# Kernel optimization log

Measured on AMD Instinct MI355X. Metric: run time of the kernel, lower is better.

The kernel has to match this reference:

```python
import jax, jax.numpy as jnp
import numpy as np

B, K, M, MN = 256, 32, 64, 256
E, H, Q = 128, 128, 128
NE, NR, NNODES = 100000, 500, 256  # entities, relations, max_nodes


def setup_inputs() -> dict:
    key = jax.random.key(0)
    ks = jax.random.split(key, 24)
    f = lambda k, s: jax.random.normal(k, s, jnp.float32) * 0.05
    inp = {}
    inp['start_entities'] = jax.random.randint(ks[0], (B,), 0, NE)
    inp['aims'] = jax.random.randint(ks[1], (B, K), 0, NE)
    inp['node_pos'] = jnp.broadcast_to(jnp.arange(1, K + 1, dtype=jnp.int32), (B, K))
    inp['neighbor_nodes'] = jax.random.randint(ks[2], (B, K, M), 0, NNODES)
    inp['neighbor_relations'] = jax.random.randint(ks[3], (B, K, M), 0, NR)
    inp['neighbors_num'] = jax.random.randint(ks[4], (B, K), 0, M + 1)
    inp['currents'] = jax.random.randint(ks[5], (B,), 0, NNODES)
    inp['candidate_nodes'] = jax.random.randint(ks[6], (B, MN), 0, NNODES)
    inp['candidate_entities'] = jax.random.randint(ks[7], (B, MN), 0, NE)
    inp['candidate_relations'] = jax.random.randint(ks[8], (B, MN), 0, NR)
    inp['candidate_masks'] = jax.random.randint(ks[9], (B, MN), 0, 2).astype(bool)
    inp['entity_emb'] = f(ks[10], (NE, E))
    inp['relation_emb'] = f(ks[11], (NR, E))
    inp['hidden_W'] = f(ks[12], (H, E)); inp['hidden_b'] = f(ks[13], (H,))
    inp['pass_W'] = f(ks[14], (H, H + E)); inp['pass_b'] = f(ks[15], (H,))
    inp['nexthop_W'] = f(ks[16], (H, H + Q)); inp['nexthop_b'] = f(ks[17], (H,))
    inp['candidate_W'] = f(ks[18], (H, H + 2 * E)); inp['candidate_b'] = f(ks[19], (H,))
    inp['gate_W'] = f(ks[20], (1, H + Q)); inp['gate_b'] = f(ks[21], (1,))
    inp['query'] = f(ks[22], (B, Q))
    return inp


def _linear(x, W, b):
    return x @ W.T + b


def _lrelu(x):
    return jax.nn.leaky_relu(x, 0.01)  # torch LeakyReLU default


def _gather_nodes(node_emb, idx):
    # node_emb: (B, N+2, H), idx: (B, ...) -> (B, ..., H)
    b = node_emb.shape[0]
    g = jnp.take_along_axis(node_emb, idx.reshape(b, -1)[:, :, None], axis=1)
    return g.reshape(*idx.shape, node_emb.shape[-1])


def reference(start_entities, aims, node_pos, neighbor_nodes, neighbor_relations,
              neighbors_num, currents, candidate_nodes, candidate_entities,
              candidate_relations, candidate_masks, entity_emb, relation_emb,
              hidden_W, hidden_b, pass_W, pass_b, nexthop_W, nexthop_b,
              candidate_W, candidate_b, gate_W, gate_b, query):
    # ---- Agent.init ----
    node_emb = jnp.zeros((B, NNODES + 2, H), jnp.float32)
    init = _lrelu(_linear(entity_emb[start_entities], hidden_W, hidden_b))
    node_emb = node_emb.at[:, 0].set(init)
    # ---- Agent.aggregate: gather -> Linear -> masked mean -> scatter ----
    aim_e = entity_emb[aims]                                   # (B,K,E)
    nb_node = _gather_nodes(node_emb, neighbor_nodes)          # (B,K,M,H)
    nb_rel = relation_emb[neighbor_relations]                  # (B,K,M,E)
    nb = _linear(jnp.concatenate([nb_node, nb_rel], -1), pass_W, pass_b)  # pass_activation = identity
    keep = jnp.arange(M) < neighbors_num[:, :, None]           # (B,K,M)
    nb = jnp.where(keep[..., None], nb, 0.0)
    denom = (neighbors_num + (neighbors_num == 0)).astype(jnp.float32)
    agg = nb.sum(axis=2) / denom[..., None]                    # (B,K,H)
    upd = _lrelu(_linear(aim_e, hidden_W, hidden_b) + agg)
    node_emb = node_emb.at[jnp.arange(B)[:, None], node_pos].set(upd)
    # ---- Agent.next_hop ----
    cur = _gather_nodes(node_emb, currents)                    # (B,H)
    cur_cat = jnp.concatenate([cur, query], axis=1)            # (B,H+Q)
    state = _lrelu(_linear(cur_cat, nexthop_W, nexthop_b))     # (B,H)
    cnode = _gather_nodes(node_emb, candidate_nodes)           # (B,MN,H)
    cand = _lrelu(_linear(jnp.concatenate(
        [cnode, entity_emb[candidate_entities], relation_emb[candidate_relations]], -1),
        candidate_W, candidate_b))                             # (B,MN,H)
    thresh = _linear(cur_cat, gate_W, gate_b)                  # (B,1)
    scores = jnp.einsum('bh,bmh->bm', state, cand) / jnp.sqrt(jnp.float32(E))
    scores = jnp.where(candidate_masks, scores, jnp.float32(-100000.0))
    final_scores = jnp.concatenate([scores, thresh], axis=1)   # (B,MN+1)
    return final_scores
```

## Files before the change

kernel.cpp:

```cpp
#include <hip/hip_runtime.h>

#define B 256
#define K 32
#define M 64
#define MN 256
#define E 128
#define H 128
#define Q 128
#define NSLOT 258
#define CTILE 32
#define XPAD 392

typedef __attribute__((ext_vector_type(8))) short short8;
typedef __attribute__((ext_vector_type(4))) short short4b;
typedef __attribute__((ext_vector_type(4))) float f32x4;

__device__ __forceinline__ float lrelu(float x){ return x >= 0.f ? x : 0.01f*x; }

__device__ __forceinline__ unsigned short f2bf(float f){
    unsigned int u = __float_as_uint(f);
    unsigned int r = u + 0x7FFFu + ((u >> 16) & 1u);
    return (unsigned short)(r >> 16);
}

__device__ __forceinline__ short4b pack4(float4 v){
    short4b r;
    r.x = (short)f2bf(v.x); r.y = (short)f2bf(v.y);
    r.z = (short)f2bf(v.z); r.w = (short)f2bf(v.w);
    return r;
}

__global__ void k_prep(const int* __restrict__ start_ent, const int* __restrict__ node_pos,
                       const float* __restrict__ ent_emb,
                       const float* __restrict__ hW, const float* __restrict__ hb,
                       const float* __restrict__ passW, const float* __restrict__ candW,
                       int* __restrict__ map,
                       float* __restrict__ init_out, float* __restrict__ wninit_out,
                       unsigned short* __restrict__ Wf, unsigned short* __restrict__ Wcatf){
    int blk = blockIdx.x, t = threadIdx.x;
    if (blk < 256) {
        int b = blk;
        __shared__ float e[E];
        __shared__ float si[H];
        if (t < 128) e[t] = ent_emb[(long)start_ent[b]*E + t];
        __syncthreads();
        if (t < 128) {
            float acc = hb[t];
            #pragma unroll 8
            for (int j=0;j<E;j++) acc += hW[t*E+j]*e[j];
            float v = lrelu(acc);
            si[t] = v;
            init_out[b*H+t] = v;
        }
        __syncthreads();
        if (t < 128) {
            float acc2 = 0.f;
            #pragma unroll 8
            for (int j=0;j<H;j++) acc2 += passW[t*(H+E)+j]*si[j];
            wninit_out[b*H+t] = acc2;
        }
    } else if (blk < 512) {
        int b = blk - 256;
        for (int i=t;i<NSLOT;i+=256) map[b*NSLOT+i] = -2;
        __syncthreads();
        if (t==0) map[b*NSLOT+0] = -1;
        __syncthreads();
        if (t<K) map[b*NSLOT + node_pos[b*K+t]] = t;
    } else if (blk < 704) {
        int i = (blk-512)*256 + t;
        int j = i & 7;
        int l = (i >> 3) & 63;
        int ct = (i >> 9) & 1;
        int r = i >> 10;
        int ks = r % 12, w = r / 12;
        int row = w*32 + ct*16 + (l & 15);
        int col = ks*32 + (l >> 4)*8 + j;
        Wf[i] = f2bf(candW[row*384 + col]);
    } else {
        int i = (blk-704)*256 + t;
        int j = i & 7;
        int l = (i >> 3) & 63;
        int ct = (i >> 9) & 1;
        int r = i >> 10;
        int ks = r & 7, w = r >> 3;
        int row = w*32 + ct*16 + (l & 15);
        int col = ks*32 + (l >> 4)*8 + j;
        float v = (col < 128) ? passW[row*256 + 128 + col] : hW[row*128 + (col-128)];
        Wcatf[i] = f2bf(v);
    }
}

__global__ void k_gather(const int* __restrict__ aims, const int* __restrict__ nbr_nodes,
                         const int* __restrict__ nbr_rels, const int* __restrict__ nbr_num,
                         const float* __restrict__ ent_emb, const float* __restrict__ rel_emb,
                         unsigned short* __restrict__ Xg,
                         float* __restrict__ ab){
    int bk = blockIdx.x;
    int t = threadIdx.x;
    int num = nbr_num[bk];
    __shared__ int sidx[M];
    __shared__ int sc0;
    __shared__ float red[8][128];
    if (t < 64) sidx[t] = nbr_rels[(long)bk*M + t];
    if (t >= 64 && t < 128) {
        int m = t - 64;
        bool flag = (m < num) && (nbr_nodes[(long)bk*M + m] == 0);
        unsigned long long mask = __ballot(flag);
        if (m == 0) sc0 = (int)__popcll(mask);
    }
    if (t >= 128) {
        int d = t - 128;
        Xg[(long)bk*256 + 128 + d] = f2bf(ent_emb[(long)aims[bk]*E + d]);
    }
    __syncthreads();
    int mg = t >> 5, q = t & 31;
    float4 acc = {0.f,0.f,0.f,0.f};
    for (int m = mg; m < num; m += 8) {
        const float4 v = *(const float4*)&rel_emb[(long)sidx[m]*E + q*4];
        acc.x += v.x; acc.y += v.y; acc.z += v.z; acc.w += v.w;
    }
    red[mg][q*4+0] = acc.x; red[mg][q*4+1] = acc.y;
    red[mg][q*4+2] = acc.z; red[mg][q*4+3] = acc.w;
    __syncthreads();
    float denom = (float)(num > 0 ? num : 1);
    if (t < 128) {
        float s = 0.f;
        #pragma unroll
        for (int g=0; g<8; g++) s += red[g][t];
        Xg[(long)bk*256 + t] = f2bf(s / denom);
    }
    if (t == 0) {
        ab[bk*2+0] = (float)sc0 / denom;
        ab[bk*2+1] = (float)num / denom;
    }
}

__global__ void k_updg(const unsigned short* __restrict__ Xg, const float* __restrict__ ab,
                       const unsigned short* __restrict__ Wcatf,
                       const float* __restrict__ hb_, const float* __restrict__ passb,
                       const float* __restrict__ wninit,
                       float* __restrict__ upd){
    int b = blockIdx.x;
    int t = threadIdx.x;
    __shared__ __align__(16) unsigned short Xs[32][264];
    __shared__ float wni[128];
    __shared__ float sab[64];
    #pragma unroll
    for (int it = 0; it < 4; it++) {
        int idx = it*256 + t;
        int r = idx >> 5;
        int cc = (idx & 31) * 8;
        *(short8*)&Xs[r][cc] = *(const short8*)&Xg[((long)b*32 + r)*256 + cc];
    }
    if (t < 128) wni[t] = wninit[b*128 + t];
    else if (t < 192) sab[t-128] = ab[b*64 + (t-128)];

    int w    = t >> 6;
    int lane = t & 63;
    int l16  = lane & 15;
    int lhi  = lane >> 4;
    int hbase = w*32;

    short8 bw[8][2];
    #pragma unroll
    for (int ks = 0; ks < 8; ks++) {
        #pragma unroll
        for (int ct = 0; ct < 2; ct++)
            bw[ks][ct] = *(const short8*)&Wcatf[((((w*8+ks)*2+ct)*64) + lane)*8];
    }
    __syncthreads();

    f32x4 acc[2][2];
    #pragma unroll
    for (int rt=0;rt<2;rt++)
        #pragma unroll
        for (int ct=0;ct<2;ct++)
            acc[rt][ct] = (f32x4){0.f,0.f,0.f,0.f};

    #pragma unroll
    for (int ks = 0; ks < 8; ks++) {
        int kof = ks*32 + lhi*8;
        short8 a0 = *(const short8*)&Xs[l16][kof];
        short8 a1 = *(const short8*)&Xs[16 + l16][kof];
        acc[0][0] = __builtin_amdgcn_mfma_f32_16x16x32_bf16(a0, bw[ks][0], acc[0][0], 0, 0, 0);
        acc[0][1] = __builtin_amdgcn_mfma_f32_16x16x32_bf16(a0, bw[ks][1], acc[0][1], 0, 0, 0);
        acc[1][0] = __builtin_amdgcn_mfma_f32_16x16x32_bf16(a1, bw[ks][0], acc[1][0], 0, 0, 0);
        acc[1][1] = __builtin_amdgcn_mfma_f32_16x16x32_bf16(a1, bw[ks][1], acc[1][1], 0, 0, 0);
    }

    int h0 = hbase + l16, h1 = hbase + 16 + l16;
    float hb0 = hb_[h0], hb1 = hb_[h1];
    float pb0 = passb[h0], pb1 = passb[h1];
    float w0 = wni[h0],  w1 = wni[h1];
    #pragma unroll
    for (int rt=0; rt<2; rt++) {
        #pragma unroll
        for (int i=0;i<4;i++) {
            int r = rt*16 + 4*lhi + i;
            float al = sab[r*2], be = sab[r*2+1];
            upd[((long)b*32 + r)*128 + h0] = lrelu(hb0 + al*w0 + be*pb0 + acc[rt][0][i]);
            upd[((long)b*32 + r)*128 + h1] = lrelu(hb1 + al*w1 + be*pb1 + acc[rt][1][i]);
        }
    }
}

__global__ void k_state(const int* __restrict__ currents, const int* __restrict__ map,
                        const float* __restrict__ init, const float* __restrict__ upd,
                        const float* __restrict__ query,
                        const float* __restrict__ nW, const float* __restrict__ nb,
                        const float* __restrict__ gW, const float* __restrict__ gb,
                        float* __restrict__ state, float* __restrict__ out){
    int b = blockIdx.x, t = threadIdx.x;
    __shared__ float cc[H+Q];
    __shared__ float wsum[2];
    int mv = map[b*NSLOT + currents[b]];
    float cv = 0.f;
    if (mv == -1) cv = init[b*H+t];
    else if (mv >= 0) cv = upd[((long)b*K+mv)*H + t];
    cc[t] = cv;
    cc[H+t] = query[b*Q+t];
    __syncthreads();
    float acc = nb[t];
    #pragma unroll 8
    for (int j=0;j<H+Q;j++) acc += nW[t*(H+Q)+j]*cc[j];
    state[b*H+t] = lrelu(acc);
    float tv = gW[t]*cc[t] + gW[H+t]*cc[H+t];
    for (int off=32; off>0; off>>=1) tv += __shfl_down(tv, off);
    if ((t&63)==0) wsum[t>>6] = tv;
    __syncthreads();
    if (t==0) out[b*(MN+1) + MN] = wsum[0] + wsum[1] + gb[0];
}

__global__ void k_cand(const int* __restrict__ cnodes, const int* __restrict__ cents,
                       const int* __restrict__ crels, const int* __restrict__ cmask,
                       const int* __restrict__ map,
                       const float* __restrict__ init, const float* __restrict__ upd,
                       const float* __restrict__ ent_emb, const float* __restrict__ rel_emb,
                       const unsigned short* __restrict__ Wf, const float* __restrict__ cb,
                       const float* __restrict__ state,
                       float* __restrict__ out){
    int blk = blockIdx.x;
    int b  = blk >> 3;
    int c0 = (blk & 7) * CTILE;
    int t  = threadIdx.x;

    __shared__ __align__(16) unsigned short Xb[CTILE][XPAD];
    __shared__ float sscore[4][CTILE];
    __shared__ int sce[CTILE], scr[CTILE], smv[CTILE];

    if (t < CTILE) {
        int row = b*MN + c0 + t;
        int cn = cnodes[row];
        sce[t] = cents[row];
        scr[t] = crels[row];
        smv[t] = map[b*NSLOT + cn];
    }
    __syncthreads();

    {
        int c8 = t >> 5;
        int q  = t & 31;
        #pragma unroll
        for (int i = 0; i < 4; i++) {
            int c = i*8 + c8;
            int mv = smv[c];
            float4 nv = {0.f,0.f,0.f,0.f};
            if (mv == -1)      nv = *(const float4*)&init[b*H + q*4];
            else if (mv >= 0)  nv = *(const float4*)&upd[((long)b*K+mv)*H + q*4];
            float4 ev = *(const float4*)&ent_emb[(long)sce[c]*E + q*4];
            float4 rv = *(const float4*)&rel_emb[(long)scr[c]*E + q*4];
            *(short4b*)&Xb[c][q*4]        = pack4(nv);
            *(short4b*)&Xb[c][128 + q*4]  = pack4(ev);
            *(short4b*)&Xb[c][256 + q*4]  = pack4(rv);
        }
    }

    int w    = t >> 6;
    int lane = t & 63;
    int l16  = lane & 15;
    int lhi  = lane >> 4;

    short8 bw[12][2];
    #pragma unroll
    for (int ks = 0; ks < 12; ks++) {
        #pragma unroll
        for (int ct = 0; ct < 2; ct++)
            bw[ks][ct] = *(const short8*)&Wf[((((w*12+ks)*2+ct)*64) + lane)*8];
    }
    float s0 = state[b*H + w*32 + l16];
    float s1 = state[b*H + w*32 + 16 + l16];
    float cb0 = cb[w*32 + l16];
    float cb1 = cb[w*32 + 16 + l16];
    __syncthreads();

    f32x4 acc[2][2];
    #pragma unroll
    for (int rt=0;rt<2;rt++)
        #pragma unroll
        for (int ct=0;ct<2;ct++)
            acc[rt][ct] = (f32x4){0.f,0.f,0.f,0.f};

    #pragma unroll
    for (int ks = 0; ks < 12; ks++) {
        int kof = ks*32 + lhi*8;
        short8 a0 = *(const short8*)&Xb[l16][kof];
        short8 a1 = *(const short8*)&Xb[16 + l16][kof];
        acc[0][0] = __builtin_amdgcn_mfma_f32_16x16x32_bf16(a0, bw[ks][0], acc[0][0], 0, 0, 0);
        acc[0][1] = __builtin_amdgcn_mfma_f32_16x16x32_bf16(a0, bw[ks][1], acc[0][1], 0, 0, 0);
        acc[1][0] = __builtin_amdgcn_mfma_f32_16x16x32_bf16(a1, bw[ks][0], acc[1][0], 0, 0, 0);
        acc[1][1] = __builtin_amdgcn_mfma_f32_16x16x32_bf16(a1, bw[ks][1], acc[1][1], 0, 0, 0);
    }

    #pragma unroll
    for (int rt=0; rt<2; rt++) {
        float ps[4];
        #pragma unroll
        for (int i=0;i<4;i++)
            ps[i] = lrelu(acc[rt][0][i] + cb0)*s0 + lrelu(acc[rt][1][i] + cb1)*s1;
        #pragma unroll
        for (int msk=1; msk<16; msk<<=1) {
            #pragma unroll
            for (int i=0;i<4;i++) ps[i] += __shfl_xor(ps[i], msk);
        }
        if (l16 == 0) {
            #pragma unroll
            for (int i=0;i<4;i++)
                sscore[w][rt*16 + 4*lhi + i] = ps[i];
        }
    }
    __syncthreads();

    if (t < CTILE) {
        int row = b*MN + c0 + t;
        float s = (sscore[0][t] + sscore[1][t] + sscore[2][t] + sscore[3][t])
                  * 0.08838834764831845f;
        out[b*(MN+1) + c0 + t] = cmask[row] ? s : -100000.0f;
    }
}

extern "C" void kernel_launch(void* const* d_in, const int* in_sizes, int n_in,
                              void* d_out, int out_size, void* d_ws, size_t ws_size,
                              hipStream_t stream){
    (void)in_sizes; (void)n_in; (void)out_size; (void)ws_size;
    const int* start_entities      = (const int*)d_in[0];
    const int* aims                = (const int*)d_in[1];
    const int* node_pos            = (const int*)d_in[2];
    const int* neighbor_nodes      = (const int*)d_in[3];
    const int* neighbor_relations  = (const int*)d_in[4];
    const int* neighbors_num       = (const int*)d_in[5];
    const int* currents            = (const int*)d_in[6];
    const int* candidate_nodes     = (const int*)d_in[7];
    const int* candidate_entities  = (const int*)d_in[8];
    const int* candidate_relations = (const int*)d_in[9];
    const int* candidate_masks     = (const int*)d_in[10];
    const float* entity_emb   = (const float*)d_in[11];
    const float* relation_emb = (const float*)d_in[12];
    const float* hidden_W     = (const float*)d_in[13];
    const float* hidden_b     = (const float*)d_in[14];
    const float* pass_W       = (const float*)d_in[15];
    const float* pass_b       = (const float*)d_in[16];
    const float* nexthop_W    = (const float*)d_in[17];
    const float* nexthop_b    = (const float*)d_in[18];
    const float* candidate_W  = (const float*)d_in[19];
    const float* candidate_b  = (const float*)d_in[20];
    const float* gate_W       = (const float*)d_in[21];
    const float* gate_b       = (const float*)d_in[22];
    const float* query        = (const float*)d_in[23];
    float* out = (float*)d_out;

    float* ws     = (float*)d_ws;
    float* init   = ws;
    float* wninit = init + B*H;
    float* upd    = wninit + B*H;
    float* state  = upd + (long)B*K*H;
    float* ab     = state + B*H;
    int*   map    = (int*)(ab + B*K*2);
    unsigned short* Wf    = (unsigned short*)(map + B*NSLOT);
    unsigned short* Wcatf = Wf + 49152;
    unsigned short* Xg    = Wcatf + 32768;

    k_prep<<<832, 256, 0, stream>>>(start_entities, node_pos, entity_emb,
                                    hidden_W, hidden_b, pass_W, candidate_W,
                                    map, init, wninit, Wf, Wcatf);
    k_gather<<<B*K, 256, 0, stream>>>(aims, neighbor_nodes, neighbor_relations, neighbors_num,
                                      entity_emb, relation_emb, Xg, ab);
    k_updg<<<B, 256, 0, stream>>>(Xg, ab, Wcatf, hidden_b, pass_b, wninit, upd);
    k_state<<<B, 128, 0, stream>>>(currents, map, init, upd, query,
                                   nexthop_W, nexthop_b, gate_W, gate_b, state, out);
    k_cand<<<B*(MN/CTILE), 256, 0, stream>>>(candidate_nodes, candidate_entities,
                                             candidate_relations, candidate_masks,
                                             map, init, upd, entity_emb, relation_emb,
                                             Wf, candidate_b, state, out);
}
```

Before: 55.90 us.

## Fuse gather into prep kernel and compute next-hop state inside candidate kernel

Merges the prep and neighbor-gather kernels into one launch. The separate next-hop state kernel is removed: each candidate block recomputes the state vector with bf16 MFMA against a pre-packed nexthop weight, and the block with c0==0 writes the gate threshold. This cuts two launches and the state round-trip through global memory. In exchange the state matvec is done redundantly in all 8 candidate blocks per batch row, and state precision drops to bf16 inputs.

```diff
diff --git a/kernel.cpp b/kernel.cpp
--- a/kernel.cpp
+++ b/kernel.cpp
@@ -30,18 +30,66 @@
     return r;
 }
 
-__global__ void k_prep(const int* __restrict__ start_ent, const int* __restrict__ node_pos,
-                       const float* __restrict__ ent_emb,
-                       const float* __restrict__ hW, const float* __restrict__ hb,
-                       const float* __restrict__ passW, const float* __restrict__ candW,
-                       int* __restrict__ map,
-                       float* __restrict__ init_out, float* __restrict__ wninit_out,
-                       unsigned short* __restrict__ Wf, unsigned short* __restrict__ Wcatf){
+__global__ void k_front(const int* __restrict__ aims, const int* __restrict__ nbr_nodes,
+                        const int* __restrict__ nbr_rels, const int* __restrict__ nbr_num,
+                        const int* __restrict__ start_ent, const int* __restrict__ node_pos,
+                        const float* __restrict__ ent_emb, const float* __restrict__ rel_emb,
+                        const float* __restrict__ hW, const float* __restrict__ hb,
+                        const float* __restrict__ passW, const float* __restrict__ nW,
+                        const float* __restrict__ candW,
+                        unsigned short* __restrict__ Xg, float* __restrict__ ab,
+                        int* __restrict__ map,
+                        float* __restrict__ init_out, float* __restrict__ wninit_out,
+                        unsigned short* __restrict__ Wf, unsigned short* __restrict__ Wcatf,
+                        unsigned short* __restrict__ nWf){
     int blk = blockIdx.x, t = threadIdx.x;
-    if (blk < 256) {
-        int b = blk;
-        __shared__ float e[E];
-        __shared__ float si[H];
+    __shared__ int sidx[M];
+    __shared__ int sc0;
+    __shared__ float red[8][128];
+
+    if (blk < B*K) {
+        int bk = blk;
+        int num = nbr_num[bk];
+        if (t < 64) sidx[t] = nbr_rels[(long)bk*M + t];
+        if (t >= 64 && t < 128) {
+            int m = t - 64;
+            bool flag = (m < num) && (nbr_nodes[(long)bk*M + m] == 0);
+            unsigned long long mask = __ballot(flag);
+            if (m == 0) sc0 = (int)__popcll(mask);
+        }
+        if (t >= 128) {
+            int d = t - 128;
+            Xg[(long)bk*256 + 128 + d] = f2bf(ent_emb[(long)aims[bk]*E + d]);
+        }
+        __syncthreads();
+        int mg = t >> 5, q = t & 31;
+        float4 acc = {0.f,0.f,0.f,0.f};
+        for (int m = mg; m < num; m += 8) {
+            const float4 v = *(const float4*)&rel_emb[(long)sidx[m]*E + q*4];
+            acc.x += v.x; acc.y += v.y; acc.z += v.z; acc.w += v.w;
+        }
+        red[mg][q*4+0] = acc.x; red[mg][q*4+1] = acc.y;
+        red[mg][q*4+2] = acc.z; red[mg][q*4+3] = acc.w;
+        __syncthreads();
+        float denom = (float)(num > 0 ? num : 1);
+        if (t < 128) {
+            float s = 0.f;
+            #pragma unroll
+            for (int g=0; g<8; g++) s += red[g][t];
+            Xg[(long)bk*256 + t] = f2bf(s / denom);
+        }
+        if (t == 0) {
+            ab[bk*2+0] = (float)sc0 / denom;
+            ab[bk*2+1] = (float)num / denom;
+        }
+        return;
+    }
+
+    int pb = blk - B*K;
+    if (pb < 256) {
+        int b = pb;
+        float* e  = red[0];
+        float* si = red[1];
         if (t < 128) e[t] = ent_emb[(long)start_ent[b]*E + t];
         __syncthreads();
         if (t < 128) {
@@ -59,15 +107,15 @@
             for (int j=0;j<H;j++) acc2 += passW[t*(H+E)+j]*si[j];
             wninit_out[b*H+t] = acc2;
         }
-    } else if (blk < 512) {
-        int b = blk - 256;
+    } else if (pb < 512) {
+        int b = pb - 256;
         for (int i=t;i<NSLOT;i+=256) map[b*NSLOT+i] = -2;
         __syncthreads();
         if (t==0) map[b*NSLOT+0] = -1;
         __syncthreads();
         if (t<K) map[b*NSLOT + node_pos[b*K+t]] = t;
-    } else if (blk < 704) {
-        int i = (blk-512)*256 + t;
+    } else if (pb < 704) {
+        int i = (pb-512)*256 + t;
         int j = i & 7;
         int l = (i >> 3) & 63;
         int ct = (i >> 9) & 1;
@@ -76,8 +124,8 @@
         int row = w*32 + ct*16 + (l & 15);
         int col = ks*32 + (l >> 4)*8 + j;
         Wf[i] = f2bf(candW[row*384 + col]);
-    } else {
-        int i = (blk-704)*256 + t;
+    } else if (pb < 832) {
+        int i = (pb-704)*256 + t;
         int j = i & 7;
         int l = (i >> 3) & 63;
         int ct = (i >> 9) & 1;
@@ -87,51 +135,16 @@
         int col = ks*32 + (l >> 4)*8 + j;
         float v = (col < 128) ? passW[row*256 + 128 + col] : hW[row*128 + (col-128)];
         Wcatf[i] = f2bf(v);
-    }
-}
-
-__global__ void k_gather(const int* __restrict__ aims, const int* __restrict__ nbr_nodes,
-                         const int* __restrict__ nbr_rels, const int* __restrict__ nbr_num,
-                         const float* __restrict__ ent_emb, const float* __restrict__ rel_emb,
-                         unsigned short* __restrict__ Xg,
-                         float* __restrict__ ab){
-    int bk = blockIdx.x;
-    int t = threadIdx.x;
-    int num = nbr_num[bk];
-    __shared__ int sidx[M];
-    __shared__ int sc0;
-    __shared__ float red[8][128];
-    if (t < 64) sidx[t] = nbr_rels[(long)bk*M + t];
-    if (t >= 64 && t < 128) {
-        int m = t - 64;
-        bool flag = (m < num) && (nbr_nodes[(long)bk*M + m] == 0);
-        unsigned long long mask = __ballot(flag);
-        if (m == 0) sc0 = (int)__popcll(mask);
-    }
-    if (t >= 128) {
-        int d = t - 128;
-        Xg[(long)bk*256 + 128 + d] = f2bf(ent_emb[(long)aims[bk]*E + d]);
-    }
-    __syncthreads();
-    int mg = t >> 5, q = t & 31;
-    float4 acc = {0.f,0.f,0.f,0.f};
-    for (int m = mg; m < num; m += 8) {
-        const float4 v = *(const float4*)&rel_emb[(long)sidx[m]*E + q*4];
-        acc.x += v.x; acc.y += v.y; acc.z += v.z; acc.w += v.w;
-    }
-    red[mg][q*4+0] = acc.x; red[mg][q*4+1] = acc.y;
-    red[mg][q*4+2] = acc.z; red[mg][q*4+3] = acc.w;
-    __syncthreads();
-    float denom = (float)(num > 0 ? num : 1);
-    if (t < 128) {
-        float s = 0.f;
-        #pragma unroll
-        for (int g=0; g<8; g++) s += red[g][t];
-        Xg[(long)bk*256 + t] = f2bf(s / denom);
-    }
-    if (t == 0) {
-        ab[bk*2+0] = (float)sc0 / denom;
-        ab[bk*2+1] = (float)num / denom;
+    } else {
+        int i = (pb-832)*256 + t;
+        int j = i & 7;
+        int l = (i >> 3) & 63;
+        int ct = (i >> 9) & 1;
+        int r = i >> 10;
+        int ks = r & 7, w = r >> 3;
+        int row = w*32 + ct*16 + (l & 15);
+        int col = ks*32 + (l >> 4)*8 + j;
+        nWf[i] = f2bf(nW[row*256 + col]);
     }
 }
 
@@ -204,40 +217,15 @@
     }
 }
 
-__global__ void k_state(const int* __restrict__ currents, const int* __restrict__ map,
-                        const float* __restrict__ init, const float* __restrict__ upd,
-                        const float* __restrict__ query,
-                        const float* __restrict__ nW, const float* __restrict__ nb,
-                        const float* __restrict__ gW, const float* __restrict__ gb,
-                        float* __restrict__ state, float* __restrict__ out){
-    int b = blockIdx.x, t = threadIdx.x;
-    __shared__ float cc[H+Q];
-    __shared__ float wsum[2];
-    int mv = map[b*NSLOT + currents[b]];
-    float cv = 0.f;
-    if (mv == -1) cv = init[b*H+t];
-    else if (mv >= 0) cv = upd[((long)b*K+mv)*H + t];
-    cc[t] = cv;
-    cc[H+t] = query[b*Q+t];
-    __syncthreads();
-    float acc = nb[t];
-    #pragma unroll 8
-    for (int j=0;j<H+Q;j++) acc += nW[t*(H+Q)+j]*cc[j];
-    state[b*H+t] = lrelu(acc);
-    float tv = gW[t]*cc[t] + gW[H+t]*cc[H+t];
-    for (int off=32; off>0; off>>=1) tv += __shfl_down(tv, off);
-    if ((t&63)==0) wsum[t>>6] = tv;
-    __syncthreads();
-    if (t==0) out[b*(MN+1) + MN] = wsum[0] + wsum[1] + gb[0];
-}
-
 __global__ void k_cand(const int* __restrict__ cnodes, const int* __restrict__ cents,
                        const int* __restrict__ crels, const int* __restrict__ cmask,
                        const int* __restrict__ map,
                        const float* __restrict__ init, const float* __restrict__ upd,
                        const float* __restrict__ ent_emb, const float* __restrict__ rel_emb,
                        const unsigned short* __restrict__ Wf, const float* __restrict__ cb,
-                       const float* __restrict__ state,
+                       const unsigned short* __restrict__ nWf, const float* __restrict__ nb_,
+                       const int* __restrict__ currents, const float* __restrict__ query,
+                       const float* __restrict__ gW, const float* __restrict__ gb,
                        float* __restrict__ out){
     int blk = blockIdx.x;
     int b  = blk >> 3;
@@ -245,6 +233,8 @@
     int t  = threadIdx.x;
 
     __shared__ __align__(16) unsigned short Xb[CTILE][XPAD];
+    __shared__ __align__(16) unsigned short ccb[256];
+    __shared__ float ccf[256];
     __shared__ float sscore[4][CTILE];
     __shared__ int sce[CTILE], scr[CTILE], smv[CTILE];
 
@@ -254,6 +244,19 @@
         sce[t] = cents[row];
         scr[t] = crels[row];
         smv[t] = map[b*NSLOT + cn];
+    } else if (t < 96) {
+        int q = t - 32;
+        float4 v;
+        if (q < 32) {
+            int mvc = map[b*NSLOT + currents[b]];
+            v = (float4){0.f,0.f,0.f,0.f};
+            if (mvc == -1)     v = *(const float4*)&init[b*H + q*4];
+            else if (mvc >= 0) v = *(const float4*)&upd[((long)b*K+mvc)*H + q*4];
+        } else {
+            v = *(const float4*)&query[b*Q + (q-32)*4];
+        }
+        *(float4*)&ccf[q*4] = v;
+        *(short4b*)&ccb[q*4] = pack4(v);
     }
     __syncthreads();
 
@@ -287,11 +290,27 @@
         for (int ct = 0; ct < 2; ct++)
             bw[ks][ct] = *(const short8*)&Wf[((((w*12+ks)*2+ct)*64) + lane)*8];
     }
-    float s0 = state[b*H + w*32 + l16];
-    float s1 = state[b*H + w*32 + 16 + l16];
     float cb0 = cb[w*32 + l16];
     float cb1 = cb[w*32 + 16 + l16];
     __syncthreads();
+
+    const short8 zero8 = (short8){0,0,0,0,0,0,0,0};
+    f32x4 accs[2];
+    accs[0] = (f32x4){0.f,0.f,0.f,0.f};
+    accs[1] = (f32x4){0.f,0.f,0.f,0.f};
+    #pragma unroll
+    for (int ks = 0; ks < 8; ks++) {
+        int kof = ks*32 + lhi*8;
+        short8 as = (l16 == 0) ? *(const short8*)&ccb[kof] : zero8;
+        short8 n0 = *(const short8*)&nWf[((((w*8+ks)*2+0)*64) + lane)*8];
+        short8 n1 = *(const short8*)&nWf[((((w*8+ks)*2+1)*64) + lane)*8];
+        accs[0] = __builtin_amdgcn_mfma_f32_16x16x32_bf16(as, n0, accs[0], 0, 0, 0);
+        accs[1] = __builtin_amdgcn_mfma_f32_16x16x32_bf16(as, n1, accs[1], 0, 0, 0);
+    }
+    float sv0 = lrelu(accs[0][0] + nb_[w*32 + l16]);
+    float sv1 = lrelu(accs[1][0] + nb_[w*32 + 16 + l16]);
+    float s0 = __shfl(sv0, l16);
+    float s1 = __shfl(sv1, l16);
 
     f32x4 acc[2][2];
     #pragma unroll
@@ -335,6 +354,13 @@
         float s = (sscore[0][t] + sscore[1][t] + sscore[2][t] + sscore[3][t])
                   * 0.08838834764831845f;
         out[b*(MN+1) + c0 + t] = cmask[row] ? s : -100000.0f;
+    }
+
+    if (c0 == 0 && t < 64) {
+        float tv = gW[t]*ccf[t] + gW[64+t]*ccf[64+t]
+                 + gW[128+t]*ccf[128+t] + gW[192+t]*ccf[192+t];
+        for (int off=32; off>0; off>>=1) tv += __shfl_down(tv, off);
+        if (t==0) out[b*(MN+1) + MN] = tv + gb[0];
     }
 }
 
@@ -372,23 +398,22 @@
     float* init   = ws;
     float* wninit = init + B*H;
     float* upd    = wninit + B*H;
-    float* state  = upd + (long)B*K*H;
-    float* ab     = state + B*H;
+    float* ab     = upd + (long)B*K*H;
     int*   map    = (int*)(ab + B*K*2);
     unsigned short* Wf    = (unsigned short*)(map + B*NSLOT);
     unsigned short* Wcatf = Wf + 49152;
-    unsigned short* Xg    = Wcatf + 32768;
-
-    k_prep<<<832, 256, 0, stream>>>(start_entities, node_pos, entity_emb,
-                                    hidden_W, hidden_b, pass_W, candidate_W,
-                                    map, init, wninit, Wf, Wcatf);
-    k_gather<<<B*K, 256, 0, stream>>>(aims, neighbor_nodes, neighbor_relations, neighbors_num,
-                                      entity_emb, relation_emb, Xg, ab);
+    unsigned short* nWf   = Wcatf + 32768;
+    unsigned short* Xg    = nWf + 32768;
+
+    k_front<<<B*K + 960, 256, 0, stream>>>(aims, neighbor_nodes, neighbor_relations,
+                                           neighbors_num, start_entities, node_pos,
+                                           entity_emb, relation_emb,
+                                           hidden_W, hidden_b, pass_W, nexthop_W, candidate_W,
+                                           Xg, ab, map, init, wninit, Wf, Wcatf, nWf);
     k_updg<<<B, 256, 0, stream>>>(Xg, ab, Wcatf, hidden_b, pass_b, wninit, upd);
-    k_state<<<B, 128, 0, stream>>>(currents, map, init, upd, query,
-                                   nexthop_W, nexthop_b, gate_W, gate_b, state, out);
     k_cand<<<B*(MN/CTILE), 256, 0, stream>>>(candidate_nodes, candidate_entities,
                                              candidate_relations, candidate_masks,
                                              map, init, upd, entity_emb, relation_emb,
-                                             Wf, candidate_b, state, out);
-}
+                                             Wf, candidate_b, nWf, nexthop_b,
+                                             currents, query, gate_W, gate_b, out);
+}
```

Measured after the change: 58.24 us. 1.04x slower.

## Merge prep and gather kernels; double-buffer candidate tiles in k_cand

Applied to the files above, without the earlier changes.

Merges the prep and neighbor-gather kernels into one launch. The gather now uses one wavefront per (b,k) pair with shuffles instead of shared-memory reductions, so one launch and one sync are gone. The candidate kernel now handles 128 candidates per block over four 32-row tiles. It loads each block's weight fragments once and prefetches the next tile's embeddings into registers while MFMAs run on the current one, using a double-buffered LDS tile. The cost is fewer blocks for the candidate stage (512 instead of 2048), more register pressure from the prefetch, and twice the LDS.

```diff
diff --git a/kernel.cpp b/kernel.cpp
--- a/kernel.cpp
+++ b/kernel.cpp
@@ -30,18 +30,61 @@
     return r;
 }
 
-__global__ void k_prep(const int* __restrict__ start_ent, const int* __restrict__ node_pos,
-                       const float* __restrict__ ent_emb,
-                       const float* __restrict__ hW, const float* __restrict__ hb,
-                       const float* __restrict__ passW, const float* __restrict__ candW,
-                       int* __restrict__ map,
-                       float* __restrict__ init_out, float* __restrict__ wninit_out,
-                       unsigned short* __restrict__ Wf, unsigned short* __restrict__ Wcatf){
+__global__ void k_front(const int* __restrict__ aims, const int* __restrict__ nbr_nodes,
+                        const int* __restrict__ nbr_rels, const int* __restrict__ nbr_num,
+                        const int* __restrict__ start_ent, const int* __restrict__ node_pos,
+                        const float* __restrict__ ent_emb, const float* __restrict__ rel_emb,
+                        const float* __restrict__ hW, const float* __restrict__ hb,
+                        const float* __restrict__ passW, const float* __restrict__ candW,
+                        unsigned short* __restrict__ Xg, float* __restrict__ ab,
+                        int* __restrict__ map,
+                        float* __restrict__ init_out, float* __restrict__ wninit_out,
+                        unsigned short* __restrict__ Wf, unsigned short* __restrict__ Wcatf){
     int blk = blockIdx.x, t = threadIdx.x;
-    if (blk < 256) {
-        int b = blk;
-        __shared__ float e[E];
-        __shared__ float si[H];
+    __shared__ float e[128];
+    __shared__ float si[128];
+
+    if (blk < (B*K)/4) {
+        int w = t >> 6, lane = t & 63;
+        int bk = blk*4 + w;
+        int num = nbr_num[bk];
+        int sidx = nbr_rels[(long)bk*M + lane];
+        int nn   = nbr_nodes[(long)bk*M + lane];
+        unsigned long long mask = __ballot((lane < num) && (nn == 0));
+        int c0 = (int)__popcll(mask);
+        float denom = (float)(num > 0 ? num : 1);
+        float ax = 0.f, ay = 0.f;
+        int m = 0;
+        for (; m + 4 <= num; m += 4) {
+            int r0 = __shfl(sidx, m+0), r1 = __shfl(sidx, m+1);
+            int r2 = __shfl(sidx, m+2), r3 = __shfl(sidx, m+3);
+            float2 v0 = *(const float2*)&rel_emb[(long)r0*E + lane*2];
+            float2 v1 = *(const float2*)&rel_emb[(long)r1*E + lane*2];
+            float2 v2 = *(const float2*)&rel_emb[(long)r2*E + lane*2];
+            float2 v3 = *(const float2*)&rel_emb[(long)r3*E + lane*2];
+            ax += v0.x + v1.x + v2.x + v3.x;
+            ay += v0.y + v1.y + v2.y + v3.y;
+        }
+        for (; m < num; ++m) {
+            int r = __shfl(sidx, m);
+            float2 v = *(const float2*)&rel_emb[(long)r*E + lane*2];
+            ax += v.x; ay += v.y;
+        }
+        ushort2 rp; rp.x = f2bf(ax/denom); rp.y = f2bf(ay/denom);
+        *(ushort2*)&Xg[(long)bk*256 + lane*2] = rp;
+        float2 av = *(const float2*)&ent_emb[(long)aims[bk]*E + lane*2];
+        ushort2 apk; apk.x = f2bf(av.x); apk.y = f2bf(av.y);
+        *(ushort2*)&Xg[(long)bk*256 + 128 + lane*2] = apk;
+        if (lane == 0) {
+            ab[bk*2+0] = (float)c0 / denom;
+            ab[bk*2+1] = (float)num / denom;
+        }
+        return;
+    }
+
+    int pb = blk - (B*K)/4;
+    if (pb < 256) {
+        int b = pb;
         if (t < 128) e[t] = ent_emb[(long)start_ent[b]*E + t];
         __syncthreads();
         if (t < 128) {
@@ -59,15 +102,15 @@
             for (int j=0;j<H;j++) acc2 += passW[t*(H+E)+j]*si[j];
             wninit_out[b*H+t] = acc2;
         }
-    } else if (blk < 512) {
-        int b = blk - 256;
+    } else if (pb < 512) {
+        int b = pb - 256;
         for (int i=t;i<NSLOT;i+=256) map[b*NSLOT+i] = -2;
         __syncthreads();
         if (t==0) map[b*NSLOT+0] = -1;
         __syncthreads();
         if (t<K) map[b*NSLOT + node_pos[b*K+t]] = t;
-    } else if (blk < 704) {
-        int i = (blk-512)*256 + t;
+    } else if (pb < 704) {
+        int i = (pb-512)*256 + t;
         int j = i & 7;
         int l = (i >> 3) & 63;
         int ct = (i >> 9) & 1;
@@ -77,7 +120,7 @@
         int col = ks*32 + (l >> 4)*8 + j;
         Wf[i] = f2bf(candW[row*384 + col]);
     } else {
-        int i = (blk-704)*256 + t;
+        int i = (pb-704)*256 + t;
         int j = i & 7;
         int l = (i >> 3) & 63;
         int ct = (i >> 9) & 1;
@@ -87,51 +130,6 @@
         int col = ks*32 + (l >> 4)*8 + j;
         float v = (col < 128) ? passW[row*256 + 128 + col] : hW[row*128 + (col-128)];
         Wcatf[i] = f2bf(v);
-    }
-}
-
-__global__ void k_gather(const int* __restrict__ aims, const int* __restrict__ nbr_nodes,
-                         const int* __restrict__ nbr_rels, const int* __restrict__ nbr_num,
-                         const float* __restrict__ ent_emb, const float* __restrict__ rel_emb,
-                         unsigned short* __restrict__ Xg,
-                         float* __restrict__ ab){
-    int bk = blockIdx.x;
-    int t = threadIdx.x;
-    int num = nbr_num[bk];
-    __shared__ int sidx[M];
-    __shared__ int sc0;
-    __shared__ float red[8][128];
-    if (t < 64) sidx[t] = nbr_rels[(long)bk*M + t];
-    if (t >= 64 && t < 128) {
-        int m = t - 64;
-        bool flag = (m < num) && (nbr_nodes[(long)bk*M + m] == 0);
-        unsigned long long mask = __ballot(flag);
-        if (m == 0) sc0 = (int)__popcll(mask);
-    }
-    if (t >= 128) {
-        int d = t - 128;
-        Xg[(long)bk*256 + 128 + d] = f2bf(ent_emb[(long)aims[bk]*E + d]);
-    }
-    __syncthreads();
-    int mg = t >> 5, q = t & 31;
-    float4 acc = {0.f,0.f,0.f,0.f};
-    for (int m = mg; m < num; m += 8) {
-        const float4 v = *(const float4*)&rel_emb[(long)sidx[m]*E + q*4];
-        acc.x += v.x; acc.y += v.y; acc.z += v.z; acc.w += v.w;
-    }
-    red[mg][q*4+0] = acc.x; red[mg][q*4+1] = acc.y;
-    red[mg][q*4+2] = acc.z; red[mg][q*4+3] = acc.w;
-    __syncthreads();
-    float denom = (float)(num > 0 ? num : 1);
-    if (t < 128) {
-        float s = 0.f;
-        #pragma unroll
-        for (int g=0; g<8; g++) s += red[g][t];
-        Xg[(long)bk*256 + t] = f2bf(s / denom);
-    }
-    if (t == 0) {
-        ab[bk*2+0] = (float)sc0 / denom;
-        ab[bk*2+1] = (float)num / denom;
     }
 }
 
@@ -240,45 +238,27 @@
                        const float* __restrict__ state,
                        float* __restrict__ out){
     int blk = blockIdx.x;
-    int b  = blk >> 3;
-    int c0 = (blk & 7) * CTILE;
+    int b  = blk >> 1;
+    int cbase = (blk & 1) * 128;
     int t  = threadIdx.x;
 
-    __shared__ __align__(16) unsigned short Xb[CTILE][XPAD];
+    __shared__ __align__(16) unsigned short Xb[2][CTILE][XPAD];
     __shared__ float sscore[4][CTILE];
-    __shared__ int sce[CTILE], scr[CTILE], smv[CTILE];
-
-    if (t < CTILE) {
-        int row = b*MN + c0 + t;
-        int cn = cnodes[row];
+    __shared__ int sce[128], scr[128], smv[128];
+
+    if (t < 128) {
+        int row = b*MN + cbase + t;
         sce[t] = cents[row];
         scr[t] = crels[row];
-        smv[t] = map[b*NSLOT + cn];
-    }
-    __syncthreads();
-
-    {
-        int c8 = t >> 5;
-        int q  = t & 31;
-        #pragma unroll
-        for (int i = 0; i < 4; i++) {
-            int c = i*8 + c8;
-            int mv = smv[c];
-            float4 nv = {0.f,0.f,0.f,0.f};
-            if (mv == -1)      nv = *(const float4*)&init[b*H + q*4];
-            else if (mv >= 0)  nv = *(const float4*)&upd[((long)b*K+mv)*H + q*4];
-            float4 ev = *(const float4*)&ent_emb[(long)sce[c]*E + q*4];
-            float4 rv = *(const float4*)&rel_emb[(long)scr[c]*E + q*4];
-            *(short4b*)&Xb[c][q*4]        = pack4(nv);
-            *(short4b*)&Xb[c][128 + q*4]  = pack4(ev);
-            *(short4b*)&Xb[c][256 + q*4]  = pack4(rv);
-        }
+        smv[t] = map[b*NSLOT + cnodes[row]];
     }
 
     int w    = t >> 6;
     int lane = t & 63;
     int l16  = lane & 15;
     int lhi  = lane >> 4;
+    int c8   = t >> 5;
+    int q    = t & 31;
 
     short8 bw[12][2];
     #pragma unroll
@@ -287,55 +267,94 @@
         for (int ct = 0; ct < 2; ct++)
             bw[ks][ct] = *(const short8*)&Wf[((((w*12+ks)*2+ct)*64) + lane)*8];
     }
-    float s0 = state[b*H + w*32 + l16];
-    float s1 = state[b*H + w*32 + 16 + l16];
+    float s0  = state[b*H + w*32 + l16];
+    float s1  = state[b*H + w*32 + 16 + l16];
     float cb0 = cb[w*32 + l16];
     float cb1 = cb[w*32 + 16 + l16];
     __syncthreads();
 
-    f32x4 acc[2][2];
-    #pragma unroll
-    for (int rt=0;rt<2;rt++)
-        #pragma unroll
-        for (int ct=0;ct<2;ct++)
-            acc[rt][ct] = (f32x4){0.f,0.f,0.f,0.f};
-
-    #pragma unroll
-    for (int ks = 0; ks < 12; ks++) {
-        int kof = ks*32 + lhi*8;
-        short8 a0 = *(const short8*)&Xb[l16][kof];
-        short8 a1 = *(const short8*)&Xb[16 + l16][kof];
-        acc[0][0] = __builtin_amdgcn_mfma_f32_16x16x32_bf16(a0, bw[ks][0], acc[0][0], 0, 0, 0);
-        acc[0][1] = __builtin_amdgcn_mfma_f32_16x16x32_bf16(a0, bw[ks][1], acc[0][1], 0, 0, 0);
-        acc[1][0] = __builtin_amdgcn_mfma_f32_16x16x32_bf16(a1, bw[ks][0], acc[1][0], 0, 0, 0);
-        acc[1][1] = __builtin_amdgcn_mfma_f32_16x16x32_bf16(a1, bw[ks][1], acc[1][1], 0, 0, 0);
-    }
-
-    #pragma unroll
-    for (int rt=0; rt<2; rt++) {
-        float ps[4];
-        #pragma unroll
-        for (int i=0;i<4;i++)
-            ps[i] = lrelu(acc[rt][0][i] + cb0)*s0 + lrelu(acc[rt][1][i] + cb1)*s1;
-        #pragma unroll
-        for (int msk=1; msk<16; msk<<=1) {
+    float4 sn[4], se[4], sr[4];
+
+#define STAGE(tile) do {                                                     \
+        _Pragma("unroll")                                                    \
+        for (int i=0;i<4;i++){                                               \
+            int ci = (tile)*32 + i*8 + c8;                                   \
+            int mv = smv[ci];                                                \
+            float4 nv = {0.f,0.f,0.f,0.f};                                   \
+            if (mv == -1)      nv = *(const float4*)&init[b*H + q*4];        \
+            else if (mv >= 0)  nv = *(const float4*)&upd[((long)b*K+mv)*H + q*4]; \
+            sn[i] = nv;                                                      \
+            se[i] = *(const float4*)&ent_emb[(long)sce[ci]*E + q*4];         \
+            sr[i] = *(const float4*)&rel_emb[(long)scr[ci]*E + q*4];         \
+        }                                                                    \
+    } while(0)
+
+#define WRITEB(buf) do {                                                     \
+        _Pragma("unroll")                                                    \
+        for (int i=0;i<4;i++){                                               \
+            int cl = i*8 + c8;                                               \
+            *(short4b*)&Xb[buf][cl][q*4]       = pack4(sn[i]);               \
+            *(short4b*)&Xb[buf][cl][128+q*4]   = pack4(se[i]);               \
+            *(short4b*)&Xb[buf][cl][256+q*4]   = pack4(sr[i]);               \
+        }                                                                    \
+    } while(0)
+
+    STAGE(0); WRITEB(0);
+    __syncthreads();
+
+    #pragma unroll
+    for (int tile = 0; tile < 4; ++tile) {
+        int cur = tile & 1;
+        if (tile < 3) STAGE(tile+1);
+
+        f32x4 acc[2][2];
+        #pragma unroll
+        for (int rt=0;rt<2;rt++)
             #pragma unroll
-            for (int i=0;i<4;i++) ps[i] += __shfl_xor(ps[i], msk);
-        }
-        if (l16 == 0) {
+            for (int ct=0;ct<2;ct++)
+                acc[rt][ct] = (f32x4){0.f,0.f,0.f,0.f};
+
+        #pragma unroll
+        for (int ks = 0; ks < 12; ks++) {
+            int kof = ks*32 + lhi*8;
+            short8 a0 = *(const short8*)&Xb[cur][l16][kof];
+            short8 a1 = *(const short8*)&Xb[cur][16 + l16][kof];
+            acc[0][0] = __builtin_amdgcn_mfma_f32_16x16x32_bf16(a0, bw[ks][0], acc[0][0], 0, 0, 0);
+            acc[0][1] = __builtin_amdgcn_mfma_f32_16x16x32_bf16(a0, bw[ks][1], acc[0][1], 0, 0, 0);
+            acc[1][0] = __builtin_amdgcn_mfma_f32_16x16x32_bf16(a1, bw[ks][0], acc[1][0], 0, 0, 0);
+            acc[1][1] = __builtin_amdgcn_mfma_f32_16x16x32_bf16(a1, bw[ks][1], acc[1][1], 0, 0, 0);
+        }
+
+        #pragma unroll
+        for (int rt=0; rt<2; rt++) {
+            float ps[4];
             #pragma unroll
             for (int i=0;i<4;i++)
-                sscore[w][rt*16 + 4*lhi + i] = ps[i];
-        }
-    }
-    __syncthreads();
-
-    if (t < CTILE) {
-        int row = b*MN + c0 + t;
-        float s = (sscore[0][t] + sscore[1][t] + sscore[2][t] + sscore[3][t])
-                  * 0.08838834764831845f;
-        out[b*(MN+1) + c0 + t] = cmask[row] ? s : -100000.0f;
-    }
+                ps[i] = lrelu(acc[rt][0][i] + cb0)*s0 + lrelu(acc[rt][1][i] + cb1)*s1;
+            #pragma unroll
+            for (int msk=1; msk<16; msk<<=1) {
+                #pragma unroll
+                for (int i=0;i<4;i++) ps[i] += __shfl_xor(ps[i], msk);
+            }
+            if (l16 == 0) {
+                #pragma unroll
+                for (int i=0;i<4;i++)
+                    sscore[w][rt*16 + 4*lhi + i] = ps[i];
+            }
+        }
+        __syncthreads();
+
+        if (t < CTILE) {
+            int row = b*MN + cbase + tile*32 + t;
+            float s = (sscore[0][t] + sscore[1][t] + sscore[2][t] + sscore[3][t])
+                      * 0.08838834764831845f;
+            out[b*(MN+1) + cbase + tile*32 + t] = cmask[row] ? s : -100000.0f;
+        }
+        if (tile < 3) WRITEB(cur^1);
+        __syncthreads();
+    }
+#undef STAGE
+#undef WRITEB
 }
 
 extern "C" void kernel_launch(void* const* d_in, const int* in_sizes, int n_in,
@@ -379,16 +398,16 @@
     unsigned short* Wcatf = Wf + 49152;
     unsigned short* Xg    = Wcatf + 32768;
 
-    k_prep<<<832, 256, 0, stream>>>(start_entities, node_pos, entity_emb,
-                                    hidden_W, hidden_b, pass_W, candidate_W,
-                                    map, init, wninit, Wf, Wcatf);
-    k_gather<<<B*K, 256, 0, stream>>>(aims, neighbor_nodes, neighbor_relations, neighbors_num,
-                                      entity_emb, relation_emb, Xg, ab);
+    k_front<<<(B*K)/4 + 832, 256, 0, stream>>>(aims, neighbor_nodes, neighbor_relations,
+                                               neighbors_num, start_entities, node_pos,
+                                               entity_emb, relation_emb,
+                                               hidden_W, hidden_b, pass_W, candidate_W,
+                                               Xg, ab, map, init, wninit, Wf, Wcatf);
     k_updg<<<B, 256, 0, stream>>>(Xg, ab, Wcatf, hidden_b, pass_b, wninit, upd);
     k_state<<<B, 128, 0, stream>>>(currents, map, init, upd, query,
                                    nexthop_W, nexthop_b, gate_W, gate_b, state, out);
-    k_cand<<<B*(MN/CTILE), 256, 0, stream>>>(candidate_nodes, candidate_entities,
-                                             candidate_relations, candidate_masks,
-                                             map, init, upd, entity_emb, relation_emb,
-                                             Wf, candidate_b, state, out);
-}
+    k_cand<<<2*B, 256, 0, stream>>>(candidate_nodes, candidate_entities,
+                                    candidate_relations, candidate_masks,
+                                    map, init, upd, entity_emb, relation_emb,
+                                    Wf, candidate_b, state, out);
+}
```

Result: slower. 90.81 us (+62.5%).
